# Performance work log

Hardware: AMD Instinct MI355X
Metric: run time of the kernel (lower is better)

## Reference

```python
import math
import jax, jax.numpy as jnp
import numpy as np

H = W = 512
FM_SIZES = [(64, 64), (32, 32), (16, 16), (8, 8), (4, 4), (2, 2)]
STEPS = [(8, 8), (16, 16), (32, 32), (64, 64), (128, 128), (256, 256)]
BOX_SIZES = [35.84, 76.8, 153.6, 230.4, 307.2, 384.0]
ASPECT_RATIOS = [1.0, 2.0, 0.5]
SCALES = [1.0, 2.0 ** (1.0 / 3.0), 2.0 ** (2.0 / 3.0)]
FG_T, BG_T = 0.6, 0.4
VAR_XY, VAR_WH = 0.1, 0.2
B, M, NUM_CLASSES = 32, 64, 10


def make_default_boxes():
    # Vectorized version of SSDBoxCoder._get_default_boxes_v2 (xywh, pixel coords)
    levels = []
    for i, (fy, fx) in enumerate(FM_SIZES):
        sy, sx = STEPS[i]
        base = BOX_SIZES[i]
        anchors = np.array(
            [[base * s * math.sqrt(ar), base * s / math.sqrt(ar)]
             for ar in ASPECT_RATIOS for s in SCALES], dtype=np.float32)  # [A,2]
        A = anchors.shape[0]
        cy = (np.arange(fy, dtype=np.float32) + 0.5) * sy
        cx = (np.arange(fx, dtype=np.float32) + 0.5) * sx
        CY, CX = np.meshgrid(cy, cx, indexing='ij')
        centers = np.stack([CX, CY], -1).reshape(-1, 1, 2)  # [fy*fx,1,2]
        lev = np.concatenate([
            np.broadcast_to(centers, (fy * fx, A, 2)),
            np.broadcast_to(anchors[None], (fy * fx, A, 2)),
        ], -1)
        levels.append(lev.reshape(-1, 4))
    return np.concatenate(levels, 0)  # [49140,4]


def xywh2xyxy(b):
    c, wh = b[..., :2], b[..., 2:]
    return jnp.concatenate([c - wh / 2, c + wh / 2], -1)


def xyxy2xywh(b):
    a, c = b[..., :2], b[..., 2:]
    return jnp.concatenate([(a + c) / 2, c - a], -1)


def box_iou(a, b):
    # a: [N,4] xyxy, b: [M,4] xyxy -> [N,M]
    lt = jnp.maximum(a[:, None, :2], b[None, :, :2])
    rb = jnp.minimum(a[:, None, 2:], b[None, :, 2:])
    wh = jnp.clip(rb - lt, 0.0)
    inter = wh[..., 0] * wh[..., 1]
    area_a = (a[:, 2] - a[:, 0]) * (a[:, 3] - a[:, 1])
    area_b = (b[:, 2] - b[:, 0]) * (b[:, 3] - b[:, 1])
    return inter / (area_a[:, None] + area_b[None, :] - inter)


def setup_inputs() -> dict:
    key = jax.random.key(0)
    k1, k2, k3 = jax.random.split(key, 3)
    cxy = jax.random.uniform(k1, (B, M, 2)) * jnp.array([W * 0.8, H * 0.8]) \
        + jnp.array([W * 0.1, H * 0.1])
    wh = jax.random.uniform(k2, (B, M, 2)) * 90.0 + 10.0
    gt_boxes = jnp.concatenate([cxy - wh / 2, cxy + wh / 2], -1)  # [B,M,4] xyxy
    labels = jax.random.randint(k3, (B, M), 0, NUM_CLASSES)
    default_boxes = jnp.asarray(make_default_boxes())  # [N,4] xywh
    return {"gt_boxes": gt_boxes, "labels": labels, "default_boxes": default_boxes}


def reference(gt_boxes, labels, default_boxes):
    db_xyxy = xywh2xyxy(default_boxes)  # [N,4]

    def encode_one(gt, lab):
        ious = box_iou(db_xyxy, gt)                 # [N,M]
        best_t = ious.max(axis=1)                   # best gt iou per prior
        best_t_idx = ious.argmax(axis=1)            # [N]
        best_p_idx = ious.argmax(axis=0)            # [M] best prior per gt
        # force-match each gt to its best prior (index_fill semantics)
        best_t_idx = best_t_idx.at[best_p_idx].set(jnp.arange(gt.shape[0]))
        best_t = best_t.at[best_p_idx].set(2.0)
        cls = (lab + 1)[best_t_idx]
        cls = jnp.where(best_t < FG_T,
                        jnp.where(best_t < BG_T, 0, -1), cls)
        b = xyxy2xywh(gt[best_t_idx])               # [N,4]
        loc_xy = (b[:, :2] - default_boxes[:, :2]) / default_boxes[:, 2:] / VAR_XY
        loc_wh = jnp.log(b[:, 2:] / default_boxes[:, 2:]) / VAR_WH
        return jnp.concatenate([loc_xy, loc_wh], 1), cls

    loc_targets, cls_targets = jax.vmap(encode_one)(gt_boxes, labels)
    return loc_targets, cls_targets
```

## Files before the change

### kernel.cpp

```cpp
#include <hip/hip_runtime.h>

#define M 64
#define FG_T 0.6f
#define BG_T 0.4f
#define PERSIST_BLOCKS 2048


__global__ __launch_bounds__(64) void lb_kernel(
    const float* __restrict__ gt,
    const float* __restrict__ db,
    float4* __restrict__ pk,
    unsigned long long* __restrict__ col)
{
#pragma clang fp contract(off)
    const int bm = blockIdx.x;
    const int t  = threadIdx.x;

    const float4 g = ((const float4*)gt)[bm];
    const float area_g = (g.z - g.x) * (g.w - g.y);
    const float gcx = (g.x + g.z) * 0.5f;
    const float gcy = (g.y + g.w) * 0.5f;

    const int   fms[6] = {64, 32, 16, 8, 4, 2};
    const float stp[6] = {8.0f, 16.0f, 32.0f, 64.0f, 128.0f, 256.0f};
    const int   off[6] = {0, 36864, 46080, 48384, 48960, 49104};

    float iou = 0.0f;
    if (t < 54) {
        const int lev = t / 9, a = t - lev * 9;
        const int fx  = fms[lev];
        int x = (int)(gcx / stp[lev]); x = min(max(x, 0), fx - 1);
        int y = (int)(gcy / stp[lev]); y = min(max(y, 0), fx - 1);
        const float4 d = ((const float4*)db)[off[lev] + (y * fx + x) * 9 + a];
        float ax0 = d.x - d.z / 2.0f;
        float ay0 = d.y - d.w / 2.0f;
        float ax1 = d.x + d.z / 2.0f;
        float ay1 = d.y + d.w / 2.0f;
        float area_a = (ax1 - ax0) * (ay1 - ay0);
        float w = fmaxf(fminf(ax1, g.z) - fmaxf(ax0, g.x), 0.0f);
        float h = fmaxf(fminf(ay1, g.w) - fmaxf(ay0, g.y), 0.0f);
        float inter = w * h;
        iou = inter / ((area_a + area_g) - inter);
    }
    #pragma unroll
    for (int o = 1; o < 64; o <<= 1) iou = fmaxf(iou, __shfl_xor(iou, o));

    if (t == 0) {
        pk[(size_t)bm * 2]     = make_float4(g.x, g.y, g.z, g.w);
        pk[(size_t)bm * 2 + 1] = make_float4(area_g, iou, 0.0f, 0.0f);
        col[bm] = 0ull;
    }
}

__global__ __launch_bounds__(256) void row_kernel(
    const float* __restrict__ gt,
    const int*   __restrict__ lab,
    const float* __restrict__ db,
    const float4* __restrict__ pk,
    float* __restrict__ out_loc,
    float* __restrict__ out_cls,
    unsigned long long* __restrict__ col,
    int N, int B, int nch)
{
#pragma clang fp contract(off)
    const int tid   = threadIdx.x;
    const int lane  = tid & 63;
    const int total = nch * B;

    for (int u = blockIdx.x; u < total; u += gridDim.x) {
        const unsigned uu = (unsigned)u;
        const int cm    = (int)(uu / (unsigned)B);
        const int b     = (int)(uu - (unsigned)cm * (unsigned)B);
        const int chunk = nch - 1 - cm;
        const int bM    = b * M;
        const float4* __restrict__ gtb = (const float4*)gt + bM;

        const int  n     = chunk * 256 + tid;
        const bool valid = (n < N);
        const int  nl    = valid ? n : (N - 1);

        const float4 d = ((const float4*)db)[nl];
        const float ax0 = d.x - d.z / 2.0f;
        const float ay0 = d.y - d.w / 2.0f;
        const float ax1 = d.x + d.z / 2.0f;
        const float ay1 = d.y + d.w / 2.0f;
        const float area_a = (ax1 - ax0) * (ay1 - ay0);

        float wx0 = ax0, wy0 = ay0, wx1 = ax1, wy1 = ay1;
        #pragma unroll
        for (int o = 1; o < 64; o <<= 1) {
            wx0 = fminf(wx0, __shfl_xor(wx0, o));
            wy0 = fminf(wy0, __shfl_xor(wy0, o));
            wx1 = fmaxf(wx1, __shfl_xor(wx1, o));
            wy1 = fmaxf(wy1, __shfl_xor(wy1, o));
        }

        const float4 gl = gtb[lane];
        const bool cand = (gl.x < wx1) && (gl.z > wx0) && (gl.y < wy1) && (gl.w > wy0);
        unsigned long long mask = __ballot((int)cand);

        float best = 0.0f;
        int   bi   = 0;

        while (mask) {
            const int m0 = __builtin_amdgcn_readfirstlane(__builtin_ctzll(mask));
            mask &= mask - 1;
            const bool has2 = (mask != 0ull);
            const int m1 = has2 ? __builtin_amdgcn_readfirstlane(__builtin_ctzll(mask)) : m0;
            if (has2) mask &= mask - 1;

            const float4 pa0 = pk[(size_t)(bM + m0) * 2];
            const float4 pb0 = pk[(size_t)(bM + m0) * 2 + 1];
            const float4 pa1 = pk[(size_t)(bM + m1) * 2];
            const float4 pb1 = pk[(size_t)(bM + m1) * 2 + 1];

            float i0 = fmaxf(fminf(ax1, pa0.z) - fmaxf(ax0, pa0.x), 0.0f)
                     * fmaxf(fminf(ay1, pa0.w) - fmaxf(ay0, pa0.y), 0.0f);
            float i1 = fmaxf(fminf(ax1, pa1.z) - fmaxf(ax0, pa1.x), 0.0f)
                     * fmaxf(fminf(ay1, pa1.w) - fmaxf(ay0, pa1.y), 0.0f);

            if (__any((i0 > 0.0f) || (i1 > 0.0f))) {
                float iou0 = i0 / ((area_a + pb0.x) - i0);
                float iou1 = i1 / ((area_a + pb1.x) - i1);

                if (iou0 > best)         { best = iou0; bi = m0; }
                if (has2 && iou1 > best) { best = iou1; bi = m1; }

                const bool c0 = valid && (iou0 >= pb0.y);
                const bool c1 = has2 && valid && (iou1 >= pb1.y);
                if (__any(c0 || c1)) {
                    if (c0) {
                        unsigned long long p =
                            (((unsigned long long)__float_as_uint(iou0)) << 32)
                            | (unsigned int)(~(unsigned int)n);
                        atomicMax(&col[bM + m0], p);
                    }
                    if (c1) {
                        unsigned long long p =
                            (((unsigned long long)__float_as_uint(iou1)) << 32)
                            | (unsigned int)(~(unsigned int)n);
                        atomicMax(&col[bM + m1], p);
                    }
                }
            }
        }

        if (valid) {
            float cv;
            if (best < BG_T)      cv = 0.0f;
            else if (best < FG_T) cv = -1.0f;
            else                  cv = (float)(lab[bM + bi] + 1);

            float4 g = gtb[bi];
            float bcx = (g.x + g.z) * 0.5f;
            float bcy = (g.y + g.w) * 0.5f;
            float bw  = g.z - g.x;
            float bh  = g.w - g.y;
            float rz  = __builtin_amdgcn_rcpf(d.z);
            float rw  = __builtin_amdgcn_rcpf(d.w);
            float lx = (bcx - d.x) * rz * 10.0f;
            float ly = (bcy - d.y) * rw * 10.0f;
            float lw = __logf(bw * rz) * 5.0f;
            float lh = __logf(bh * rw) * 5.0f;

            ((float4*)out_loc)[(size_t)b * N + n] = make_float4(lx, ly, lw, lh);
            out_cls[(size_t)b * N + n] = cv;
        }
    }
}

__global__ void fixup_kernel(
    const float* __restrict__ gt,
    const int*   __restrict__ lab,
    const float* __restrict__ db,
    const unsigned long long* __restrict__ col,
    float* __restrict__ out_loc,
    float* __restrict__ out_cls,
    int N)
{
#pragma clang fp contract(off)
    __shared__ int s_a[M];
    const int b = blockIdx.x;
    const int m = threadIdx.x;

    unsigned long long p = col[b * M + m];
    int a = (p == 0ull) ? 0 : (int)(~(unsigned int)(p & 0xFFFFFFFFull));
    a = min(max(a, 0), N - 1);
    s_a[m] = a;
    __syncthreads();

    bool write = true;
    for (int mm = m + 1; mm < M; ++mm) {
        if (s_a[mm] == a) { write = false; break; }
    }
    if (write) {
        float4 d = ((const float4*)db)[a];
        float4 g = ((const float4*)gt)[b * M + m];
        float bcx = (g.x + g.z) / 2.0f;
        float bcy = (g.y + g.w) / 2.0f;
        float bw  = g.z - g.x;
        float bh  = g.w - g.y;
        float lx = ((bcx - d.x) / d.z) / 0.1f;
        float ly = ((bcy - d.y) / d.w) / 0.1f;
        float lw = __logf(bw / d.z) / 0.2f;
        float lh = __logf(bh / d.w) / 0.2f;

        ((float4*)out_loc)[(size_t)b * N + a] = make_float4(lx, ly, lw, lh);
        out_cls[(size_t)b * N + a] = (float)(lab[b * M + m] + 1);
    }
}

extern "C" void kernel_launch(void* const* d_in, const int* in_sizes, int n_in,
                              void* d_out, int out_size, void* d_ws, size_t ws_size,
                              hipStream_t stream) {
    const float* gt  = (const float*)d_in[0];
    const int*   lab = (const int*)d_in[1];
    const float* db  = (const float*)d_in[2];

    const int B = in_sizes[1] / M;
    const int N = in_sizes[2] / 4;
    const int nch = (N + 255) / 256;

    float* out_loc = (float*)d_out;
    float* out_cls = out_loc + (size_t)B * N * 4;

    unsigned long long* col = (unsigned long long*)d_ws;
    float4*             pkp = (float4*)(col + (size_t)B * M);

    const int total = nch * B;
    const int grid  = total < PERSIST_BLOCKS ? total : PERSIST_BLOCKS;

    lb_kernel<<<dim3(B * M), dim3(64), 0, stream>>>(gt, db, pkp, col);
    row_kernel<<<dim3(grid), dim3(256), 0, stream>>>(
        gt, lab, db, pkp, out_loc, out_cls, col, N, B, nch);
    fixup_kernel<<<dim3(B), dim3(M), 0, stream>>>(gt, lab, db, col, out_loc, out_cls, N);
}
```

Measured before the change: 99.00 us.

## Precompute per-wave candidate masks in first kernel and unroll candidate loop by four

Candidate-GT bitmasks are now computed once per 64-prior wave tile and per batch image inside lb_kernel, and stored in workspace. row_kernel reads the precomputed mask instead of doing a shuffle reduction of the prior bounding window and a ballot on every iteration. The candidate loop also processes four GT boxes per step instead of two, giving more memory-level parallelism on the pk loads. The cost is a larger lb_kernel, which loops over all batches per wave tile, plus extra workspace traffic for the masks.

Result: slower. 109.6 us (+10.7%).

```diff
diff --git a/kernel.cpp b/kernel.cpp
--- a/kernel.cpp
+++ b/kernel.cpp
@@ -10,45 +10,77 @@
     const float* __restrict__ gt,
     const float* __restrict__ db,
     float4* __restrict__ pk,
-    unsigned long long* __restrict__ col)
+    unsigned long long* __restrict__ col,
+    unsigned long long* __restrict__ masks,
+    int N, int B, int nch)
 {
 #pragma clang fp contract(off)
     const int bm = blockIdx.x;
     const int t  = threadIdx.x;
 
-    const float4 g = ((const float4*)gt)[bm];
-    const float area_g = (g.z - g.x) * (g.w - g.y);
-    const float gcx = (g.x + g.z) * 0.5f;
-    const float gcy = (g.y + g.w) * 0.5f;
-
-    const int   fms[6] = {64, 32, 16, 8, 4, 2};
-    const float stp[6] = {8.0f, 16.0f, 32.0f, 64.0f, 128.0f, 256.0f};
-    const int   off[6] = {0, 36864, 46080, 48384, 48960, 49104};
-
-    float iou = 0.0f;
-    if (t < 54) {
-        const int lev = t / 9, a = t - lev * 9;
-        const int fx  = fms[lev];
-        int x = (int)(gcx / stp[lev]); x = min(max(x, 0), fx - 1);
-        int y = (int)(gcy / stp[lev]); y = min(max(y, 0), fx - 1);
-        const float4 d = ((const float4*)db)[off[lev] + (y * fx + x) * 9 + a];
-        float ax0 = d.x - d.z / 2.0f;
-        float ay0 = d.y - d.w / 2.0f;
-        float ax1 = d.x + d.z / 2.0f;
-        float ay1 = d.y + d.w / 2.0f;
-        float area_a = (ax1 - ax0) * (ay1 - ay0);
-        float w = fmaxf(fminf(ax1, g.z) - fmaxf(ax0, g.x), 0.0f);
-        float h = fmaxf(fminf(ay1, g.w) - fmaxf(ay0, g.y), 0.0f);
-        float inter = w * h;
-        iou = inter / ((area_a + area_g) - inter);
-    }
-    #pragma unroll
-    for (int o = 1; o < 64; o <<= 1) iou = fmaxf(iou, __shfl_xor(iou, o));
-
-    if (t == 0) {
-        pk[(size_t)bm * 2]     = make_float4(g.x, g.y, g.z, g.w);
-        pk[(size_t)bm * 2 + 1] = make_float4(area_g, iou, 0.0f, 0.0f);
-        col[bm] = 0ull;
+    {
+        const float4 g = ((const float4*)gt)[bm];
+        const float area_g = (g.z - g.x) * (g.w - g.y);
+        const float gcx = (g.x + g.z) * 0.5f;
+        const float gcy = (g.y + g.w) * 0.5f;
+
+        const int   fms[6] = {64, 32, 16, 8, 4, 2};
+        const float stp[6] = {8.0f, 16.0f, 32.0f, 64.0f, 128.0f, 256.0f};
+        const int   off[6] = {0, 36864, 46080, 48384, 48960, 49104};
+
+        float iou = 0.0f;
+        if (t < 54) {
+            const int lev = t / 9, a = t - lev * 9;
+            const int fx  = fms[lev];
+            int x = (int)(gcx / stp[lev]); x = min(max(x, 0), fx - 1);
+            int y = (int)(gcy / stp[lev]); y = min(max(y, 0), fx - 1);
+            const float4 d = ((const float4*)db)[off[lev] + (y * fx + x) * 9 + a];
+            float ax0 = d.x - d.z / 2.0f;
+            float ay0 = d.y - d.w / 2.0f;
+            float ax1 = d.x + d.z / 2.0f;
+            float ay1 = d.y + d.w / 2.0f;
+            float area_a = (ax1 - ax0) * (ay1 - ay0);
+            float w = fmaxf(fminf(ax1, g.z) - fmaxf(ax0, g.x), 0.0f);
+            float h = fmaxf(fminf(ay1, g.w) - fmaxf(ay0, g.y), 0.0f);
+            float inter = w * h;
+            iou = inter / ((area_a + area_g) - inter);
+        }
+        #pragma unroll
+        for (int o = 1; o < 64; o <<= 1) iou = fmaxf(iou, __shfl_xor(iou, o));
+
+        if (t == 0) {
+            pk[(size_t)bm * 2]     = make_float4(g.x, g.y, g.z, g.w);
+            pk[(size_t)bm * 2 + 1] = make_float4(area_g, iou, 0.0f, 0.0f);
+            col[bm] = 0ull;
+        }
+    }
+
+    const int nch4 = nch * 4;
+    for (int cw = blockIdx.x; cw < nch4; cw += gridDim.x) {
+        const int n  = cw * 64 + t;
+        const int nl = (n < N) ? n : (N - 1);
+        const float4 d = ((const float4*)db)[nl];
+        const float ax0 = d.x - d.z / 2.0f;
+        const float ay0 = d.y - d.w / 2.0f;
+        const float ax1 = d.x + d.z / 2.0f;
+        const float ay1 = d.y + d.w / 2.0f;
+
+        float wx0 = ax0, wy0 = ay0, wx1 = ax1, wy1 = ay1;
+        #pragma unroll
+        for (int o = 1; o < 64; o <<= 1) {
+            wx0 = fminf(wx0, __shfl_xor(wx0, o));
+            wy0 = fminf(wy0, __shfl_xor(wy0, o));
+            wx1 = fmaxf(wx1, __shfl_xor(wx1, o));
+            wy1 = fmaxf(wy1, __shfl_xor(wy1, o));
+        }
+
+        for (int b = 0; b < B; ++b) {
+            const float4 gl = ((const float4*)gt)[b * M + t];
+            const bool cand = (gl.x < wx1) && (gl.z > wx0) &&
+                              (gl.y < wy1) && (gl.w > wy0);
+            const unsigned long long mk = __ballot((int)cand);
+            if (t == 0) masks[(size_t)cw * B + b] = mk;
+        }
     }
 }
 
@@ -57,6 +89,7 @@
     const int*   __restrict__ lab,
     const float* __restrict__ db,
     const float4* __restrict__ pk,
+    const unsigned long long* __restrict__ masks,
     float* __restrict__ out_loc,
     float* __restrict__ out_cls,
     unsigned long long* __restrict__ col,
@@ -64,7 +97,6 @@
 {
 #pragma clang fp contract(off)
     const int tid   = threadIdx.x;
-    const int lane  = tid & 63;
     const int total = nch * B;
 
     for (int u = blockIdx.x; u < total; u += gridDim.x) {
@@ -86,18 +118,8 @@
         const float ay1 = d.y + d.w / 2.0f;
         const float area_a = (ax1 - ax0) * (ay1 - ay0);
 
-        float wx0 = ax0, wy0 = ay0, wx1 = ax1, wy1 = ay1;
-        #pragma unroll
-        for (int o = 1; o < 64; o <<= 1) {
-            wx0 = fminf(wx0, __shfl_xor(wx0, o));
-            wy0 = fminf(wy0, __shfl_xor(wy0, o));
-            wx1 = fmaxf(wx1, __shfl_xor(wx1, o));
-            wy1 = fmaxf(wy1, __shfl_xor(wy1, o));
-        }
-
-        const float4 gl = gtb[lane];
-        const bool cand = (gl.x < wx1) && (gl.z > wx0) && (gl.y < wy1) && (gl.w > wy0);
-        unsigned long long mask = __ballot((int)cand);
+        const int cw = __builtin_amdgcn_readfirstlane((chunk << 2) | (tid >> 6));
+        unsigned long long mask = masks[(size_t)cw * B + b];
 
         float best = 0.0f;
         int   bi   = 0;
@@ -105,30 +127,50 @@
         while (mask) {
             const int m0 = __builtin_amdgcn_readfirstlane(__builtin_ctzll(mask));
             mask &= mask - 1;
-            const bool has2 = (mask != 0ull);
-            const int m1 = has2 ? __builtin_amdgcn_readfirstlane(__builtin_ctzll(mask)) : m0;
-            if (has2) mask &= mask - 1;
+            const bool h1 = (mask != 0ull);
+            const int  m1 = h1 ? __builtin_amdgcn_readfirstlane(__builtin_ctzll(mask)) : m0;
+            if (h1) mask &= mask - 1;
+            const bool h2 = (mask != 0ull);
+            const int  m2 = h2 ? __builtin_amdgcn_readfirstlane(__builtin_ctzll(mask)) : m0;
+            if (h2) mask &= mask - 1;
+            const bool h3 = (mask != 0ull);
+            const int  m3 = h3 ? __builtin_amdgcn_readfirstlane(__builtin_ctzll(mask)) : m0;
+            if (h3) mask &= mask - 1;
 
             const float4 pa0 = pk[(size_t)(bM + m0) * 2];
             const float4 pb0 = pk[(size_t)(bM + m0) * 2 + 1];
             const float4 pa1 = pk[(size_t)(bM + m1) * 2];
             const float4 pb1 = pk[(size_t)(bM + m1) * 2 + 1];
+            const float4 pa2 = pk[(size_t)(bM + m2) * 2];
+            const float4 pb2 = pk[(size_t)(bM + m2) * 2 + 1];
+            const float4 pa3 = pk[(size_t)(bM + m3) * 2];
+            const float4 pb3 = pk[(size_t)(bM + m3) * 2 + 1];
 
             float i0 = fmaxf(fminf(ax1, pa0.z) - fmaxf(ax0, pa0.x), 0.0f)
                      * fmaxf(fminf(ay1, pa0.w) - fmaxf(ay0, pa0.y), 0.0f);
             float i1 = fmaxf(fminf(ax1, pa1.z) - fmaxf(ax0, pa1.x), 0.0f)
                      * fmaxf(fminf(ay1, pa1.w) - fmaxf(ay0, pa1.y), 0.0f);
-
-            if (__any((i0 > 0.0f) || (i1 > 0.0f))) {
+            float i2 = fmaxf(fminf(ax1, pa2.z) - fmaxf(ax0, pa2.x), 0.0f)
+                     * fmaxf(fminf(ay1, pa2.w) - fmaxf(ay0, pa2.y), 0.0f);
+            float i3 = fmaxf(fminf(ax1, pa3.z) - fmaxf(ax0, pa3.x), 0.0f)
+                     * fmaxf(fminf(ay1, pa3.w) - fmaxf(ay0, pa3.y), 0.0f);
+
+            if (__any((i0 > 0.0f) || (i1 > 0.0f) || (i2 > 0.0f) || (i3 > 0.0f))) {
                 float iou0 = i0 / ((area_a + pb0.x) - i0);
                 float iou1 = i1 / ((area_a + pb1.x) - i1);
-
-                if (iou0 > best)         { best = iou0; bi = m0; }
-                if (has2 && iou1 > best) { best = iou1; bi = m1; }
+                float iou2 = i2 / ((area_a + pb2.x) - i2);
+                float iou3 = i3 / ((area_a + pb3.x) - i3);
+
+                if (iou0 > best)       { best = iou0; bi = m0; }
+                if (h1 && iou1 > best) { best = iou1; bi = m1; }
+                if (h2 && iou2 > best) { best = iou2; bi = m2; }
+                if (h3 && iou3 > best) { best = iou3; bi = m3; }
 
                 const bool c0 = valid && (iou0 >= pb0.y);
-                const bool c1 = has2 && valid && (iou1 >= pb1.y);
-                if (__any(c0 || c1)) {
+                const bool c1 = h1 && valid && (iou1 >= pb1.y);
+                const bool c2 = h2 && valid && (iou2 >= pb2.y);
+                const bool c3 = h3 && valid && (iou3 >= pb3.y);
+                if (__any(c0 || c1 || c2 || c3)) {
                     if (c0) {
                         unsigned long long p =
                             (((unsigned long long)__float_as_uint(iou0)) << 32)
@@ -140,6 +182,18 @@
                             (((unsigned long long)__float_as_uint(iou1)) << 32)
                             | (unsigned int)(~(unsigned int)n);
                         atomicMax(&col[bM + m1], p);
+                    }
+                    if (c2) {
+                        unsigned long long p =
+                            (((unsigned long long)__float_as_uint(iou2)) << 32)
+                            | (unsigned int)(~(unsigned int)n);
+                        atomicMax(&col[bM + m2], p);
+                    }
+                    if (c3) {
+                        unsigned long long p =
+                            (((unsigned long long)__float_as_uint(iou3)) << 32)
+                            | (unsigned int)(~(unsigned int)n);
+                        atomicMax(&col[bM + m3], p);
                     }
                 }
             }
@@ -226,12 +280,13 @@
 
     unsigned long long* col = (unsigned long long*)d_ws;
     float4*             pkp = (float4*)(col + (size_t)B * M);
+    unsigned long long* msk = (unsigned long long*)(pkp + (size_t)B * M * 2);
 
     const int total = nch * B;
     const int grid  = total < PERSIST_BLOCKS ? total : PERSIST_BLOCKS;
 
-    lb_kernel<<<dim3(B * M), dim3(64), 0, stream>>>(gt, db, pkp, col);
+    lb_kernel<<<dim3(B * M), dim3(64), 0, stream>>>(gt, db, pkp, col, msk, N, B, nch);
     row_kernel<<<dim3(grid), dim3(256), 0, stream>>>(
-        gt, lab, db, pkp, out_loc, out_cls, col, N, B, nch);
+        gt, lab, db, pkp, msk, out_loc, out_cls, col, N, B, nch);
     fixup_kernel<<<dim3(B), dim3(M), 0, stream>>>(gt, lab, db, col, out_loc, out_cls, N);
 }
```
